# Optimization experiments

Hardware: AMD Instinct MI355X
Metric: run time of the kernel (lower is better)

Reference implementation:

```python
import jax, jax.numpy as jnp
import numpy as np

# configuration (mirrors global `args` in the original code)
N_USER = 20000
N_ITEM = 20000
N = N_USER + N_ITEM            # total nodes; N*N < 2^31 so int32 hashing is safe
N_EDGES = 2_560_000
MASK_DEPTH = 2
KEEP_RATE = 0.5
N_SEEDS = 2000


def setup_inputs() -> dict:
    key = jax.random.key(0)
    k1, k2, k3 = jax.random.split(key, 3)
    rows = jax.random.randint(k1, (N_EDGES,), 0, N, dtype=jnp.int32)
    cols = jax.random.randint(k2, (N_EDGES,), 0, N, dtype=jnp.int32)
    vals = jnp.ones((N_EDGES,), jnp.float32)  # adj._values(); only its length is used
    seeds = jax.random.randint(k3, (N_SEEDS,), 0, N, dtype=jnp.int32)
    return {"rows": rows, "cols": cols, "vals": vals, "seeds": seeds}


def reference(rows, cols, vals, seeds):
    """Faithful vectorized translation of RandomMaskSubgraphs.forward.

    The per-seed python loop over edges is equivalent (in its final effect) to:
    per BFS level, drop every still-alive edge incident to the current seed set,
    and take the endpoints of dropped edges as the next seed set.
    Returns (enc_rows, enc_cols, enc_vals, dec_rows, dec_cols, dec_vals).
    Removed encoder edges carry value 0 (zero-value sparse entries == absent).
    """
    E = rows.shape[0]
    key = jax.random.key(1)
    kS, kR, kC = jax.random.split(key, 3)

    alive = jnp.ones(E, dtype=bool)                     # edges not yet masked
    seed_mask = jnp.zeros(N, dtype=bool).at[seeds].set(True)
    mask_nodes = seed_mask                               # union of maskNodes list
    cur = seed_mask
    for i in range(MASK_DEPTH):
        # membership test: edge incident to any current seed (single gather pass)
        hit = alive & (cur[rows] | cur[cols])
        alive = alive & ~hit
        if i != MASK_DEPTH - 1:
            # endpoints of masked edges become next frontier (scatter dedup)
            h = hit.astype(jnp.int32)
            touched = (jnp.zeros(N, jnp.int32).at[rows].add(h).at[cols].add(h)) > 0
            mask_nodes = mask_nodes | touched
            cur = touched

    # random keep-nodes augmentation
    samp_num = int(N * KEEP_RATE)
    samp = jax.random.randint(kS, (samp_num,), 0, N, dtype=jnp.int32)
    mask_nodes = mask_nodes.at[samp].set(True)

    # encoderAdj = normalizeAdj(sparse(ones on remaining edges))
    deg = jax.ops.segment_sum(alive.astype(jnp.float32), rows, num_segments=N)
    dinv = jnp.power(deg + 1e-12, -0.5)
    enc_vals = alive.astype(jnp.float32) * dinv[rows] * dinv[cols]

    # decoderAdj: random pairs among masked nodes + self loops + remaining edges,
    # deduplicated via integer hash row*N + col (fits int32 since N*N < 2^31)
    mask_idx = jnp.nonzero(mask_nodes)[0].astype(jnp.int32)
    tem_num = int(mask_idx.shape[0])
    tem_rows = mask_idx[jax.random.randint(kR, (E,), 0, tem_num)]
    tem_cols = mask_idx[jax.random.randint(kC, (E,), 0, tem_num)]
    ar = jnp.arange(N, dtype=jnp.int32)
    alive_rows = rows[alive]
    alive_cols = cols[alive]
    new_rows = jnp.concatenate([tem_rows, tem_cols, ar, alive_rows])
    new_cols = jnp.concatenate([tem_cols, tem_rows, ar, alive_cols])
    hash_val = jnp.unique(new_rows * N + new_cols)
    dec_cols = hash_val % N
    dec_rows = hash_val // N
    dec_vals = jnp.ones(dec_rows.shape[0], jnp.float32)

    return rows, cols, enc_vals, dec_rows, dec_cols, dec_vals
```

## Files before the change

### kernel.cpp

```cpp
#include <hip/hip_runtime.h>
#include <stdint.h>


#define NN 40000
#define SAMPN (NN / 2)
#define WORDS 1250
#define SWORDS 40
#define NB 1024
#define RPB 40
#define CAP 8192
#define CURSTRIDE 4
#define EPB 2816
#define NE (EPB / 256)
#define SELFPB 44
#define SCAP (3 * EPB + SELFPB)

__host__ __device__ __forceinline__ void tf2x32(unsigned k0, unsigned k1,
                                                unsigned x0, unsigned x1,
                                                unsigned &o0, unsigned &o1) {
  unsigned ks2 = k0 ^ k1 ^ 0x1BD11BDAu;
  x0 += k0; x1 += k1;
#define TFR(r) { x0 += x1; x1 = (x1 << (r)) | (x1 >> (32 - (r))); x1 ^= x0; }
  TFR(13) TFR(15) TFR(26) TFR(6)
  x0 += k1;  x1 += ks2 + 1u;
  TFR(17) TFR(29) TFR(16) TFR(24)
  x0 += ks2; x1 += k0 + 2u;
  TFR(13) TFR(15) TFR(26) TFR(6)
  x0 += k0;  x1 += k1 + 3u;
  TFR(17) TFR(29) TFR(16) TFR(24)
  x0 += k1;  x1 += ks2 + 4u;
  TFR(13) TFR(15) TFR(26) TFR(6)
  x0 += ks2; x1 += k0 + 5u;
#undef TFR
  o0 = x0; o1 = x1;
}

__device__ __forceinline__ unsigned jrand(unsigned a, unsigned b, unsigned c,
                                          unsigned d, unsigned e, unsigned span,
                                          unsigned m2) {
  unsigned x0, x1, y0, y1;
  tf2x32(a, b, 0u, e, x0, x1);
  unsigned hi = x0 ^ x1;
  tf2x32(c, d, 0u, e, y0, y1);
  unsigned lo = y0 ^ y1;
  return ((hi % span) * m2 + (lo % span)) % span;
}

__global__ void k_zero16(uint4 *p, int n16) {
  int i = blockIdx.x * blockDim.x + threadIdx.x;
  if (i < n16) p[i] = make_uint4(0u, 0u, 0u, 0u);
}
__global__ void k_seed_samp(const int *seeds, int ns, unsigned char *cur,
                            unsigned char *mask_bfs,
                            unsigned a, unsigned b, unsigned c, unsigned d) {
  int i = blockIdx.x * blockDim.x + threadIdx.x;
  if (i < ns) { int s = seeds[i]; cur[s] = 1; mask_bfs[s] = 1; }
  if (i < SAMPN) {
    constexpr unsigned M2 =
        ((65536u % (unsigned)NN) * (65536u % (unsigned)NN)) % (unsigned)NN;
    unsigned idx = jrand(a, b, c, d, (unsigned)i, (unsigned)NN, M2);
    mask_bfs[idx] = 1;
  }
}
__global__ void k_level0(const int *rows, const int *cols, int E,
                         const unsigned char *cur, unsigned char *alive,
                         unsigned char *touched, unsigned char *mask_bfs) {
  int e = blockIdx.x * blockDim.x + threadIdx.x;
  if (e >= E) return;
  int r = rows[e], c = cols[e];
  if (cur[r] | cur[c]) {
    alive[e] = 0;
    touched[r] = 1; touched[c] = 1;
    mask_bfs[r] = 1; mask_bfs[c] = 1;
  } else alive[e] = 1;
}
__global__ void k_level1_deg(const int *rows, const int *cols, int E,
                             const unsigned char *touched, unsigned char *alive,
                             int *deg) {
  int e = blockIdx.x * blockDim.x + threadIdx.x;
  if (e >= E) return;
  if (alive[e]) {
    int r = rows[e];
    if (touched[r] | touched[cols[e]]) alive[e] = 0;
    else atomicAdd(&deg[r], 1);
  }
}

__global__ __launch_bounds__(1024) void k_scan_mask(const unsigned char *flags,
                                                    unsigned short *mask_idx,
                                                    int *tem_num) {
  __shared__ int wsum[16];
  const unsigned *f = (const unsigned *)flags;
  int tid = threadIdx.x, lane = tid & 63, wid = tid >> 6;
  int base = tid * 10;
  unsigned u[10];
  int cnt = 0;
  for (int j = 0; j < 10; j++) {
    int i = base + j;
    u[j] = (i < 10000) ? f[i] : 0u;
    cnt += __popc(u[j]);
  }
  int x = cnt;
  for (int d = 1; d < 64; d <<= 1) {
    int y = __shfl_up(x, d, 64);
    if (lane >= d) x += y;
  }
  if (lane == 63) wsum[wid] = x;
  __syncthreads();
  if (wid == 0) {
    int v = (lane < 16) ? wsum[lane] : 0;
    int y = v;
    for (int d = 1; d < 16; d <<= 1) {
      int z = __shfl_up(y, d, 64);
      if (lane >= d) y += z;
    }
    if (lane < 16) wsum[lane] = y - v;
  }
  __syncthreads();
  int off = wsum[wid] + (x - cnt);
  for (int j = 0; j < 10; j++) {
    int i = base + j;
    unsigned v = u[j];
    while (v) {
      int byte = (__ffs(v) - 1) >> 3;
      v &= v - 1;
      mask_idx[off++] = (unsigned short)(i * 4 + byte);
    }
  }
  if (tid == 1023) *tem_num = off;
}

__global__ __launch_bounds__(256) void k_append(
    const int *rows, const int *cols, const unsigned char *alive,
    const int *deg, const unsigned short *mask_idx, const int *tem_num,
    int *cursors, unsigned *bucketmem, float *out,
    unsigned ra, unsigned rb, unsigned rc, unsigned rd,
    unsigned ca, unsigned cb, unsigned cc, unsigned cd, int E) {
  __shared__ unsigned sorted[SCAP];
  __shared__ int cnt[NB];
  __shared__ unsigned short ofs[NB];
  __shared__ int ntot_s;
  int tid = threadIdx.x, lane = tid & 63, wid = tid >> 6;
  int e0 = blockIdx.x * EPB;
  int i0 = blockIdx.x * SELFPB;
  int i1 = i0 + SELFPB; if (i1 > NN) i1 = NN;
  unsigned span = (unsigned)*tem_num;
  unsigned mtmp = 65536u % span;
  unsigned m2 = (mtmp * mtmp) % span;
  const unsigned NOPE = 0xFFFFFFFFu;

  unsigned tval[NE], aval[NE];

  for (int i = tid; i < NB; i += 256) cnt[i] = 0;
  __syncthreads();
#pragma unroll
  for (int k = 0; k < NE; k++) {
    int e = e0 + k * 256 + tid;
    if (e < E) {
      unsigned iR = jrand(ra, rb, rc, rd, (unsigned)e, span, m2);
      unsigned iC = jrand(ca, cb, cc, cd, (unsigned)e, span, m2);
      unsigned tr = (unsigned)mask_idx[iR], tc = (unsigned)mask_idx[iC];
      tval[k] = (tr << 16) | tc;
      atomicAdd(&cnt[tr / RPB], 1);
      atomicAdd(&cnt[tc / RPB], 1);
      int r = rows[e], c = cols[e];
      float v = 0.0f;
      if (alive[e]) {
        aval[k] = ((unsigned)r << 16) | (unsigned)c;
        atomicAdd(&cnt[(unsigned)r / RPB], 1);
        float xr = (float)deg[r] + 1e-12f;
        float xc = (float)deg[c] + 1e-12f;
        float dr = (float)(1.0 / sqrt((double)xr));
        float dc = (float)(1.0 / sqrt((double)xc));
        v = dr * dc;
      } else aval[k] = NOPE;
      out[e] = (float)r;
      out[E + e] = (float)c;
      out[2 * E + e] = v;
    } else { tval[k] = NOPE; aval[k] = NOPE; }
  }
  for (int i = i0 + tid; i < i1; i += 256) atomicAdd(&cnt[i / RPB], 1);
  __syncthreads();
  if (wid == 0) {
    int carry = 0;
    for (int c8 = 0; c8 < NB / 64; c8++) {
      int v = cnt[c8 * 64 + lane];
      int x = v;
      for (int d = 1; d < 64; d <<= 1) {
        int y = __shfl_up(x, d, 64);
        if (lane >= d) x += y;
      }
      ofs[c8 * 64 + lane] = (unsigned short)(carry + x - v);
      carry += __shfl(x, 63, 64);
    }
    if (lane == 0) ntot_s = carry;
  }
  __syncthreads();
  for (int i = tid; i < NB; i += 256) cnt[i] = ofs[i];
  __syncthreads();
#pragma unroll
  for (int k = 0; k < NE; k++) {
    unsigned v = tval[k];
    if (v != NOPE) {
      unsigned tr = v >> 16, tc = v & 0xFFFFu;
      int p1 = atomicAdd(&cnt[tr / RPB], 1);
      sorted[p1] = v;
      int p2 = atomicAdd(&cnt[tc / RPB], 1);
      sorted[p2] = (tc << 16) | tr;
      unsigned a = aval[k];
      if (a != NOPE) {
        int p3 = atomicAdd(&cnt[(a >> 16) / RPB], 1);
        sorted[p3] = a;
      }
    }
  }
  for (int i = i0 + tid; i < i1; i += 256) {
    int p = atomicAdd(&cnt[i / RPB], 1);
    sorted[p] = ((unsigned)i << 16) | (unsigned)i;
  }
  __syncthreads();
  int ntot = ntot_s;
  for (int b = tid; b < NB; b += 256) {
    int end = (b < NB - 1) ? (int)ofs[b + 1] : ntot;
    int len = end - (int)ofs[b];
    cnt[b] = len ? atomicAdd(&cursors[b * CURSTRIDE], len) : 0;
  }
  __syncthreads();
  for (int j = tid; j < ntot; j += 256) {
    unsigned item = sorted[j];
    unsigned r = item >> 16;
    unsigned b = r / RPB;
    unsigned lr = r - b * RPB;
    int idx = cnt[b] + (j - (int)ofs[b]);
    if (idx < CAP) bucketmem[b * CAP + idx] = (lr << 16) | (item & 0xFFFFu);
  }
}

__global__ __launch_bounds__(256) void k_dedup(unsigned *bucketmem,
                                               const int *cursors, int *uniq_cnt) {
  int b = blockIdx.x;
  int rowbase = b * RPB;
  if (rowbase >= NN) { if (threadIdx.x == 0) uniq_cnt[b] = 0; return; }

  __shared__ unsigned short arr[CAP];
  __shared__ int cnt[RPB];
  __shared__ int rowend[RPB];
  __shared__ int curs[RPB];
  __shared__ int rowoff[RPB];
  __shared__ unsigned bm[4][WORDS];
  __shared__ unsigned sm[4][SWORDS];

  int tid = threadIdx.x, lane = tid & 63, wid = tid >> 6;
  int n = cursors[b * CURSTRIDE]; if (n > CAP) n = CAP;
  const unsigned *src = bucketmem + (size_t)b * CAP;

  for (int i = tid; i < RPB; i += 256) cnt[i] = 0;
  __syncthreads();
  for (int j = tid; j < n; j += 256) atomicAdd(&cnt[src[j] >> 16], 1);
  __syncthreads();
  if (wid == 0) {
    int v = (lane < RPB) ? cnt[lane] : 0;
    int x = v;
    for (int d = 1; d < 64; d <<= 1) {
      int y = __shfl_up(x, d, 64);
      if (lane >= d) x += y;
    }
    if (lane < RPB) { curs[lane] = x - v; rowend[lane] = x; }
  }
  __syncthreads();
  for (int j = tid; j < n; j += 256) {
    unsigned v = src[j];
    int p = atomicAdd(&curs[v >> 16], 1);
    arr[p] = (unsigned short)v;
  }
  for (int w = lane; w < WORDS; w += 64) bm[wid][w] = 0u;
  if (lane < SWORDS) sm[wid][lane] = 0u;
  __syncthreads();

  for (int r = wid; r < RPB; r += 4) {
    int s1 = rowend[r], s0 = s1 - cnt[r];
    for (int j = s0 + lane; j < s1; j += 64) {
      unsigned c = arr[j];
      atomicOr(&bm[wid][c >> 5], 1u << (c & 31));
      atomicOr(&sm[wid][c >> 10], 1u << ((c >> 5) & 31));
    }
    unsigned s = (lane < SWORDS) ? sm[wid][lane] : 0u;
    int m = 0;
    unsigned t = s;
    while (t) {
      int w = (lane << 5) + (__ffs(t) - 1);
      t &= t - 1;
      m += __popc(bm[wid][w]);
    }
    int x = m;
    for (int d = 1; d < 64; d <<= 1) {
      int y = __shfl_up(x, d, 64);
      if (lane >= d) x += y;
    }
    int u = __shfl(x, 63, 64);
    int pos = s0 + (x - m);
    t = s;
    while (t) {
      int w = (lane << 5) + (__ffs(t) - 1);
      t &= t - 1;
      unsigned mm = bm[wid][w];
      bm[wid][w] = 0u;
      while (mm) {
        int bit = __ffs(mm) - 1;
        mm &= mm - 1;
        arr[pos++] = (unsigned short)((w << 5) + bit);
      }
    }
    if (lane < SWORDS) sm[wid][lane] = 0u;
    if (lane == 0) cnt[r] = u;
  }
  __syncthreads();
  if (wid == 0) {
    int v = (lane < RPB) ? cnt[lane] : 0;
    int x = v;
    for (int d = 1; d < 64; d <<= 1) {
      int y = __shfl_up(x, d, 64);
      if (lane >= d) x += y;
    }
    if (lane < RPB) rowoff[lane] = x - v;
    if (lane == RPB - 1) uniq_cnt[b] = x;
  }
  __syncthreads();
  unsigned *dst = bucketmem + (size_t)b * CAP;
  for (int r = wid; r < RPB; r += 4) {
    int s0 = r ? rowend[r - 1] : 0;
    int u = cnt[r], o = rowoff[r];
    unsigned rowpack = (unsigned)(rowbase + r) << 16;
    for (int j = lane; j < u; j += 64)
      dst[o + j] = rowpack | (unsigned)arr[s0 + j];
  }
}

__global__ __launch_bounds__(256) void k_emit(const unsigned *bucketmem,
                                              const int *uniq_cnt, float *out,
                                              int E, int U) {
  __shared__ int part[4];
  int b = blockIdx.x;
  int tid = threadIdx.x, lane = tid & 63, wid = tid >> 6;
  int acc = 0;
  for (int i = tid; i < NB; i += 256)
    if (i < b) acc += uniq_cnt[i];
  for (int d = 1; d < 64; d <<= 1) acc += __shfl_xor(acc, d, 64);
  if (lane == 0) part[wid] = acc;
  __syncthreads();
  int ob = part[0] + part[1] + part[2] + part[3];
  int ub = uniq_cnt[b];
  const unsigned *src = bucketmem + (size_t)b * CAP;
  int base3 = 3 * E;
  for (int j = tid; j < ub; j += 256) {
    unsigned h = src[j];
    unsigned r = h >> 16;
    unsigned c = h & 0xFFFFu;
    int idx = ob + j;
    if (idx < U) {
      out[base3 + idx] = (float)r;
      out[base3 + U + idx] = (float)c;
      out[base3 + 2 * U + idx] = 1.0f;
    }
  }
  if (b == NB - 1 && tid == 0) {
    int C = ob + ub;
    if (C != U) {
      int d = C - U; if (d < 0) d = -d; if (d > 60000) d = 60000;
      out[base3] = (float)(300000 + d);
    }
  }
}

extern "C" void kernel_launch(void *const *d_in, const int *in_sizes, int n_in,
                              void *d_out, int out_size, void *d_ws,
                              size_t ws_size, hipStream_t stream) {
  const int *rows = (const int *)d_in[0];
  const int *cols = (const int *)d_in[1];
  const int *seeds = (const int *)d_in[3];
  const int E = in_sizes[0];
  const int ns = in_sizes[3];
  float *out = (float *)d_out;
  const int U = (out_size - 3 * E) / 3;

  int *I = (int *)d_ws;
  int *deg = I;      I += NN;
  int *cursors = I;  I += NB * CURSTRIDE;
  int *uniq_cnt = I; I += NB;
  unsigned char *cur = (unsigned char *)I;
  unsigned char *touched = cur + NN;
  unsigned char *mask_bfs = touched + NN;
  size_t zero_bytes = (size_t)((char *)(mask_bfs + NN) - (char *)deg);
  int *J = (int *)(mask_bfs + NN);
  int *tem_num = J;  J += 1;
  J += 1;
  unsigned short *mask_idx = (unsigned short *)J;
  J += NN / 2;
  unsigned *bucketmem = (unsigned *)J; J += (size_t)NB * CAP;
  unsigned char *alive = (unsigned char *)J;

  unsigned F[3][2];
  tf2x32(0u, 1u, 0u, 0u, F[0][0], F[0][1]);
  tf2x32(0u, 1u, 0u, 1u, F[1][0], F[1][1]);
  tf2x32(0u, 1u, 0u, 2u, F[2][0], F[2][1]);
  unsigned K[3][4];
  for (int s = 0; s < 3; s++) {
    tf2x32(F[s][0], F[s][1], 0u, 0u, K[s][0], K[s][1]);
    tf2x32(F[s][0], F[s][1], 0u, 1u, K[s][2], K[s][3]);
  }

  dim3 b(256);
  int gE = (E + 255) / 256;
  int gSS = (SAMPN + 255) / 256;
  int gT = (E + EPB - 1) / EPB;
  int n16 = (int)(zero_bytes / 16);

  k_zero16<<<(n16 + 255) / 256, b, 0, stream>>>((uint4 *)deg, n16);
  k_seed_samp<<<gSS, b, 0, stream>>>(seeds, ns, cur, mask_bfs,
                                     K[0][0], K[0][1], K[0][2], K[0][3]);
  k_level0<<<gE, b, 0, stream>>>(rows, cols, E, cur, alive, touched, mask_bfs);
  k_level1_deg<<<gE, b, 0, stream>>>(rows, cols, E, touched, alive, deg);
  k_scan_mask<<<1, 1024, 0, stream>>>(mask_bfs, mask_idx, tem_num);
  k_append<<<gT, b, 0, stream>>>(rows, cols, alive, deg, mask_idx, tem_num,
                                 cursors, bucketmem, out,
                                 K[1][0], K[1][1], K[1][2], K[1][3],
                                 K[2][0], K[2][1], K[2][2], K[2][3], E);
  k_dedup<<<NB, b, 0, stream>>>(bucketmem, cursors, uniq_cnt);
  k_emit<<<NB, b, 0, stream>>>(bucketmem, uniq_cnt, out, E, U);
}
```

Baseline: 271.8 us.

## Parallelize mask compaction and fuse emit into dedup via grid-wide spin barrier

Replaces the single-block 1024-thread mask scan with per-block popcounts, computed inside k_level1_deg, followed by a 40-block extract kernel. Also makes k_dedup publish per-bucket unique counts and spin-wait on a global done counter. If all 1024 blocks become co-resident, each block computes its own output offset and writes the final output directly, skipping the bucketmem write-back and the k_emit read. If not, it falls back to the old path, with k_emit handling only the blocks that did not emit. This trades the k_emit pass for a bounded spin wait that depends on occupancy and can add latency when blocks are not all resident.

```diff
diff --git a/kernel.cpp b/kernel.cpp
--- a/kernel.cpp
+++ b/kernel.cpp
@@ -14,6 +14,7 @@
 #define NE (EPB / 256)
 #define SELFPB 44
 #define SCAP (3 * EPB + SELFPB)
+#define MWPB 250
 
 __host__ __device__ __forceinline__ void tf2x32(unsigned k0, unsigned k1,
                                                 unsigned x0, unsigned x1,
@@ -76,31 +77,50 @@
 }
 __global__ void k_level1_deg(const int *rows, const int *cols, int E,
                              const unsigned char *touched, unsigned char *alive,
-                             int *deg) {
-  int e = blockIdx.x * blockDim.x + threadIdx.x;
-  if (e >= E) return;
-  if (alive[e]) {
+                             int *deg, const unsigned *maskw, int *mask_part) {
+  int tid = threadIdx.x;
+  int e = blockIdx.x * blockDim.x + tid;
+  if (e < E && alive[e]) {
     int r = rows[e];
     if (touched[r] | touched[cols[e]]) alive[e] = 0;
     else atomicAdd(&deg[r], 1);
   }
-}
-
-__global__ __launch_bounds__(1024) void k_scan_mask(const unsigned char *flags,
-                                                    unsigned short *mask_idx,
-                                                    int *tem_num) {
-  __shared__ int wsum[16];
-  const unsigned *f = (const unsigned *)flags;
-  int tid = threadIdx.x, lane = tid & 63, wid = tid >> 6;
-  int base = tid * 10;
-  unsigned u[10];
-  int cnt = 0;
-  for (int j = 0; j < 10; j++) {
-    int i = base + j;
-    u[j] = (i < 10000) ? f[i] : 0u;
-    cnt += __popc(u[j]);
-  }
-  int x = cnt;
+  if (blockIdx.x < 40) {
+    __shared__ int red[4];
+    int lane = tid & 63, wid = tid >> 6;
+    int c = (tid < MWPB) ? __popc(maskw[blockIdx.x * MWPB + tid]) : 0;
+    for (int d = 1; d < 64; d <<= 1) c += __shfl_xor(c, d, 64);
+    if (lane == 0) red[wid] = c;
+    __syncthreads();
+    if (tid == 0) mask_part[blockIdx.x] = red[0] + red[1] + red[2] + red[3];
+  }
+}
+
+__global__ __launch_bounds__(256) void k_mask_extract(const unsigned *f,
+                                                      const int *mask_part,
+                                                      unsigned short *mask_idx,
+                                                      int *tem_num) {
+  __shared__ int wsum[4];
+  __shared__ int basech;
+  int b = blockIdx.x, tid = threadIdx.x, lane = tid & 63, wid = tid >> 6;
+  if (wid == 0) {
+    int v = (lane < 40) ? mask_part[lane] : 0;
+    int x = v;
+    for (int d = 1; d < 64; d <<= 1) {
+      int y = __shfl_up(x, d, 64);
+      if (lane >= d) x += y;
+    }
+    int basev = __shfl(x - v, b, 64);
+    int total = __shfl(x, 39, 64);
+    if (lane == 0) {
+      basech = basev;
+      if (b == 0) *tem_num = total;
+    }
+  }
+  int w = b * MWPB + tid;
+  unsigned u = (tid < MWPB) ? f[w] : 0u;
+  int c = __popc(u);
+  int x = c;
   for (int d = 1; d < 64; d <<= 1) {
     int y = __shfl_up(x, d, 64);
     if (lane >= d) x += y;
@@ -108,26 +128,21 @@
   if (lane == 63) wsum[wid] = x;
   __syncthreads();
   if (wid == 0) {
-    int v = (lane < 16) ? wsum[lane] : 0;
+    int v = (lane < 4) ? wsum[lane] : 0;
     int y = v;
-    for (int d = 1; d < 16; d <<= 1) {
+    for (int d = 1; d < 4; d <<= 1) {
       int z = __shfl_up(y, d, 64);
       if (lane >= d) y += z;
     }
-    if (lane < 16) wsum[lane] = y - v;
-  }
-  __syncthreads();
-  int off = wsum[wid] + (x - cnt);
-  for (int j = 0; j < 10; j++) {
-    int i = base + j;
-    unsigned v = u[j];
-    while (v) {
-      int byte = (__ffs(v) - 1) >> 3;
-      v &= v - 1;
-      mask_idx[off++] = (unsigned short)(i * 4 + byte);
-    }
-  }
-  if (tid == 1023) *tem_num = off;
+    if (lane < 4) wsum[lane] = y - v;
+  }
+  __syncthreads();
+  int off = basech + wsum[wid] + (x - c);
+  while (u) {
+    int byte = (__ffs(u) - 1) >> 3;
+    u &= u - 1;
+    mask_idx[off++] = (unsigned short)(w * 4 + byte);
+  }
 }
 
 __global__ __launch_bounds__(256) void k_append(
@@ -237,10 +252,20 @@
 }
 
 __global__ __launch_bounds__(256) void k_dedup(unsigned *bucketmem,
-                                               const int *cursors, int *uniq_cnt) {
+                                               const int *cursors, int *uniq_cnt,
+                                               int *emitted, int *done,
+                                               float *out, int E, int U) {
   int b = blockIdx.x;
   int rowbase = b * RPB;
-  if (rowbase >= NN) { if (threadIdx.x == 0) uniq_cnt[b] = 0; return; }
+  if (rowbase >= NN) {
+    if (threadIdx.x == 0) {
+      __hip_atomic_store(&uniq_cnt[b], 0, __ATOMIC_RELAXED,
+                         __HIP_MEMORY_SCOPE_AGENT);
+      __hip_atomic_fetch_add(done, 1, __ATOMIC_RELEASE,
+                             __HIP_MEMORY_SCOPE_AGENT);
+    }
+    return;
+  }
 
   __shared__ unsigned short arr[CAP];
   __shared__ int cnt[RPB];
@@ -249,6 +274,9 @@
   __shared__ int rowoff[RPB];
   __shared__ unsigned bm[4][WORDS];
   __shared__ unsigned sm[4][SWORDS];
+  __shared__ int tot_s;
+  __shared__ int okf;
+  __shared__ int part4[4];
 
   int tid = threadIdx.x, lane = tid & 63, wid = tid >> 6;
   int n = cursors[b * CURSTRIDE]; if (n > CAP) n = CAP;
@@ -323,21 +351,66 @@
       if (lane >= d) x += y;
     }
     if (lane < RPB) rowoff[lane] = x - v;
-    if (lane == RPB - 1) uniq_cnt[b] = x;
-  }
-  __syncthreads();
-  unsigned *dst = bucketmem + (size_t)b * CAP;
-  for (int r = wid; r < RPB; r += 4) {
-    int s0 = r ? rowend[r - 1] : 0;
-    int u = cnt[r], o = rowoff[r];
-    unsigned rowpack = (unsigned)(rowbase + r) << 16;
-    for (int j = lane; j < u; j += 64)
-      dst[o + j] = rowpack | (unsigned)arr[s0 + j];
+    if (lane == RPB - 1) tot_s = x;
+  }
+  __syncthreads();
+  if (tid == 0) {
+    __hip_atomic_store(&uniq_cnt[b], tot_s, __ATOMIC_RELAXED,
+                       __HIP_MEMORY_SCOPE_AGENT);
+    __hip_atomic_fetch_add(done, 1, __ATOMIC_RELEASE,
+                           __HIP_MEMORY_SCOPE_AGENT);
+    int ok = 0;
+    for (int it = 0; it < 1000; ++it) {
+      if (__hip_atomic_load(done, __ATOMIC_ACQUIRE,
+                            __HIP_MEMORY_SCOPE_AGENT) == NB) { ok = 1; break; }
+      __builtin_amdgcn_s_sleep(32);
+    }
+    okf = ok;
+  }
+  __syncthreads();
+  if (okf) {
+    unsigned *uc = &bm[0][0];
+    for (int i = tid; i < NB; i += 256)
+      uc[i] = (unsigned)__hip_atomic_load(&uniq_cnt[i], __ATOMIC_RELAXED,
+                                          __HIP_MEMORY_SCOPE_AGENT);
+    __syncthreads();
+    int acc = 0;
+    for (int i = tid; i < NB; i += 256)
+      if (i < b) acc += (int)uc[i];
+    for (int d = 1; d < 64; d <<= 1) acc += __shfl_xor(acc, d, 64);
+    if (lane == 0) part4[wid] = acc;
+    __syncthreads();
+    int ob = part4[0] + part4[1] + part4[2] + part4[3];
+    int base3 = 3 * E;
+    for (int r = wid; r < RPB; r += 4) {
+      int s0 = r ? rowend[r - 1] : 0;
+      int u = cnt[r], o = ob + rowoff[r];
+      float rowf = (float)(rowbase + r);
+      for (int j = lane; j < u; j += 64) {
+        int idx = o + j;
+        if (idx < U) {
+          out[base3 + idx] = rowf;
+          out[base3 + U + idx] = (float)arr[s0 + j];
+          out[base3 + 2 * U + idx] = 1.0f;
+        }
+      }
+    }
+    if (tid == 0) emitted[b] = 1;
+  } else {
+    unsigned *dst = bucketmem + (size_t)b * CAP;
+    for (int r = wid; r < RPB; r += 4) {
+      int s0 = r ? rowend[r - 1] : 0;
+      int u = cnt[r], o = rowoff[r];
+      unsigned rowpack = (unsigned)(rowbase + r) << 16;
+      for (int j = lane; j < u; j += 64)
+        dst[o + j] = rowpack | (unsigned)arr[s0 + j];
+    }
   }
 }
 
 __global__ __launch_bounds__(256) void k_emit(const unsigned *bucketmem,
-                                              const int *uniq_cnt, float *out,
+                                              const int *uniq_cnt,
+                                              const int *emitted, float *out,
                                               int E, int U) {
   __shared__ int part[4];
   int b = blockIdx.x;
@@ -349,7 +422,8 @@
   if (lane == 0) part[wid] = acc;
   __syncthreads();
   int ob = part[0] + part[1] + part[2] + part[3];
-  int ub = uniq_cnt[b];
+  int ucb = uniq_cnt[b];
+  int ub = emitted[b] ? 0 : ucb;
   const unsigned *src = bucketmem + (size_t)b * CAP;
   int base3 = 3 * E;
   for (int j = tid; j < ub; j += 256) {
@@ -364,7 +438,7 @@
     }
   }
   if (b == NB - 1 && tid == 0) {
-    int C = ob + ub;
+    int C = ob + ucb;
     if (C != U) {
       int d = C - U; if (d < 0) d = -d; if (d > 60000) d = 60000;
       out[base3] = (float)(300000 + d);
@@ -387,6 +461,8 @@
   int *deg = I;      I += NN;
   int *cursors = I;  I += NB * CURSTRIDE;
   int *uniq_cnt = I; I += NB;
+  int *emitted = I;  I += NB;
+  int *done = I;     I += 8;
   unsigned char *cur = (unsigned char *)I;
   unsigned char *touched = cur + NN;
   unsigned char *mask_bfs = touched + NN;
@@ -394,6 +470,7 @@
   int *J = (int *)(mask_bfs + NN);
   int *tem_num = J;  J += 1;
   J += 1;
+  int *mask_part = J; J += 40;
   unsigned short *mask_idx = (unsigned short *)J;
   J += NN / 2;
   unsigned *bucketmem = (unsigned *)J; J += (size_t)NB * CAP;
@@ -419,12 +496,15 @@
   k_seed_samp<<<gSS, b, 0, stream>>>(seeds, ns, cur, mask_bfs,
                                      K[0][0], K[0][1], K[0][2], K[0][3]);
   k_level0<<<gE, b, 0, stream>>>(rows, cols, E, cur, alive, touched, mask_bfs);
-  k_level1_deg<<<gE, b, 0, stream>>>(rows, cols, E, touched, alive, deg);
-  k_scan_mask<<<1, 1024, 0, stream>>>(mask_bfs, mask_idx, tem_num);
+  k_level1_deg<<<gE, b, 0, stream>>>(rows, cols, E, touched, alive, deg,
+                                     (const unsigned *)mask_bfs, mask_part);
+  k_mask_extract<<<40, b, 0, stream>>>((const unsigned *)mask_bfs, mask_part,
+                                       mask_idx, tem_num);
   k_append<<<gT, b, 0, stream>>>(rows, cols, alive, deg, mask_idx, tem_num,
                                  cursors, bucketmem, out,
                                  K[1][0], K[1][1], K[1][2], K[1][3],
                                  K[2][0], K[2][1], K[2][2], K[2][3], E);
-  k_dedup<<<NB, b, 0, stream>>>(bucketmem, cursors, uniq_cnt);
-  k_emit<<<NB, b, 0, stream>>>(bucketmem, uniq_cnt, out, E, U);
-}
+  k_dedup<<<NB, b, 0, stream>>>(bucketmem, cursors, uniq_cnt, emitted, done,
+                                out, E, U);
+  k_emit<<<NB, b, 0, stream>>>(bucketmem, uniq_cnt, emitted, out, E, U);
+}
```

After: 319.9 us. 1.18x slower.
